# Optimization experiments

Measured on AMD Instinct MI355X. Metric: run time of the kernel, lower is better.

The kernel has to match this reference:

```python
import jax, jax.numpy as jnp
import numpy as np


def setup_inputs() -> dict:
    key = jax.random.key(0)
    ks = jax.random.split(key, 8)
    B, IN, H, OUT = 8192, 1024, 2048, 1024
    SIGMA_MIN, SIGMA_MAX, PHASE = 0.9, 0.999, 2.0 * np.pi
    # recurrence decay params, initialized as in the torch module
    rng = np.random.RandomState(0)
    u1 = rng.random_sample(H)
    u2 = rng.random_sample(H)
    v = -0.5 * np.log(u1 * (SIGMA_MAX ** 2 - SIGMA_MIN ** 2) + SIGMA_MIN ** 2)
    theta = u2 * PHASE
    scale_b = 1.0 / np.sqrt(IN)
    scale_c = 1.0 / np.sqrt(H)
    return {
        "x": jax.random.normal(ks[0], (B, IN), dtype=jnp.float32),
        "h_prev": jax.random.normal(ks[1], (B, H), dtype=jnp.float32),
        "Br": jax.random.normal(ks[2], (H, IN), dtype=jnp.float32) * scale_b,
        "Bi": jax.random.normal(ks[3], (H, IN), dtype=jnp.float32) * scale_b,
        "Cr": jax.random.normal(ks[4], (OUT, H), dtype=jnp.float32) * scale_c,
        "Ci": jax.random.normal(ks[5], (OUT, H), dtype=jnp.float32) * scale_c,
        "v_log": jnp.asarray(np.log(v), dtype=jnp.float32),
        "theta_log": jnp.asarray(np.log(theta), dtype=jnp.float32),
    }


def reference(x, h_prev, Br, Bi, Cr, Ci, v_log, theta_log):
    # effective diagonal recurrence weight w = exp(-exp(v_log) + i*exp(theta_log))
    mag = jnp.exp(-jnp.exp(v_log))            # [H]
    ang = jnp.exp(theta_log)                  # [H]
    wr = mag * jnp.cos(ang)
    wi = mag * jnp.sin(ang)
    # h = B(x) + h_prev * w  (h_prev is real -> imag part comes only from wi)
    # complexLinear on real x: real = x@Br^T, imag = x@Bi^T
    hr = jnp.einsum('bi,hi->bh', x, Br) + h_prev * wr   # [B,H]
    hi = jnp.einsum('bi,hi->bh', x, Bi) + h_prev * wi   # [B,H]
    # out = Re(C(h)) = hr@Cr^T - hi@Ci^T
    out = jnp.einsum('bh,oh->bo', hr, Cr) - jnp.einsum('bh,oh->bo', hi, Ci)
    return out
```

## Files before the change

### kernel.cpp

```cpp
#include <hip/hip_runtime.h>
#include <stdint.h>

typedef unsigned short u16;
typedef short bf16x8 __attribute__((ext_vector_type(8)));
typedef float f32x4 __attribute__((ext_vector_type(4)));

typedef void as1_void __attribute__((address_space(1)));
typedef void as3_void __attribute__((address_space(3)));

__device__ inline u16 f32_to_bf16(float f) {
    uint32_t u = __builtin_bit_cast(uint32_t, f);
    u += 0x7fffu + ((u >> 16) & 1u);
    return (u16)(u >> 16);
}

__device__ inline void gld_lds16(const void* g, void* l) {
    __builtin_amdgcn_global_load_lds((as1_void*)g, (as3_void*)l, 16, 0, 0);
}


__global__ void prep_w_kernel(const float* __restrict__ v_log,
                              const float* __restrict__ theta_log,
                              float* __restrict__ wfull, int H) {
    int h = blockIdx.x * blockDim.x + threadIdx.x;
    if (h < H) {
        float mag = expf(-expf(v_log[h]));
        float ang = expf(theta_log[h]);
        wfull[h]     = mag * cosf(ang);
        wfull[h + H] = mag * sinf(ang);
    }
}

__global__ void pack_ccat_kernel(const float* __restrict__ Cr,
                                 const float* __restrict__ Ci,
                                 u16* __restrict__ Ccat, int total4) {
    int i = blockIdx.x * blockDim.x + threadIdx.x;
    if (i >= total4) return;
    int e = i * 4;
    int o = e >> 12;
    int k = e & 4095;
    float4 f; float s;
    if (k < 2048) { f = *(const float4*)(Cr + (size_t)o * 2048 + k);          s =  1.f; }
    else          { f = *(const float4*)(Ci + (size_t)o * 2048 + (k - 2048)); s = -1.f; }
    ushort4 u;
    u.x = f32_to_bf16(s * f.x); u.y = f32_to_bf16(s * f.y);
    u.z = f32_to_bf16(s * f.z); u.w = f32_to_bf16(s * f.w);
    ((ushort4*)Ccat)[i] = u;
}

__global__ void transpose_cast_kernel(const float* __restrict__ Br,
                                      const float* __restrict__ Bi,
                                      u16* __restrict__ Bcat) {
    __shared__ float t[32][33];
    const float* src = blockIdx.z ? Bi : Br;
    int colOff = blockIdx.z ? 2048 : 0;
    int c0 = blockIdx.x * 32, r0 = blockIdx.y * 32;
    int tx = threadIdx.x, ty = threadIdx.y;
#pragma unroll
    for (int j = 0; j < 4; j++)
        t[ty + j * 8][tx] = src[(size_t)(r0 + ty + j * 8) * 1024 + c0 + tx];
    __syncthreads();
#pragma unroll
    for (int j = 0; j < 4; j++)
        Bcat[(size_t)(c0 + ty + j * 8) * 4096 + colOff + r0 + tx] =
            f32_to_bf16(t[tx][ty + j * 8]);
}

__global__ void cast_f32_bf16_kernel(const float* __restrict__ src,
                                     u16* __restrict__ dst, int n4) {
    int i = blockIdx.x * blockDim.x + threadIdx.x;
    if (i < n4) {
        float4 f = ((const float4*)src)[i];
        ushort4 o;
        o.x = f32_to_bf16(f.x); o.y = f32_to_bf16(f.y);
        o.z = f32_to_bf16(f.z); o.w = f32_to_bf16(f.w);
        ((ushort4*)dst)[i] = o;
    }
}

__global__ void reduce_cw_kernel(const float* __restrict__ partials,
                                 const float* __restrict__ Cr, const float* __restrict__ Ci,
                                 const float* __restrict__ wfull,
                                 u16* __restrict__ Wmain, u16* __restrict__ Cwbf) {
    const int n4_red = 1024 * 1024 / 4;
    const int n4_cw  = 1024 * 2048 / 4;
    int i = blockIdx.x * blockDim.x + threadIdx.x;
    if (i < n4_red) {
        int e = i * 4;
        float4 s = *(const float4*)(partials + e);
#pragma unroll
        for (int z = 1; z < 4; z++) {
            float4 p = *(const float4*)(partials + ((size_t)z << 20) + e);
            s.x += p.x; s.y += p.y; s.z += p.z; s.w += p.w;
        }
        ushort4 u;
        u.x = f32_to_bf16(s.x); u.y = f32_to_bf16(s.y);
        u.z = f32_to_bf16(s.z); u.w = f32_to_bf16(s.w);
        ((ushort4*)Wmain)[i] = u;
    } else if (i < n4_red + n4_cw) {
        int j = i - n4_red;
        int e = j * 4;
        int o = e >> 11;
        int h = e & 2047;
        float4 cr = *(const float4*)(Cr + (size_t)o * 2048 + h);
        float4 ci = *(const float4*)(Ci + (size_t)o * 2048 + h);
        float4 wr = *(const float4*)(wfull + h);
        float4 wi = *(const float4*)(wfull + 2048 + h);
        ushort4 u;
        u.x = f32_to_bf16(cr.x * wr.x - ci.x * wi.x);
        u.y = f32_to_bf16(cr.y * wr.y - ci.y * wi.y);
        u.z = f32_to_bf16(cr.z * wr.z - ci.z * wi.z);
        u.w = f32_to_bf16(cr.w * wr.w - ci.w * wi.w);
        ((ushort4*)Cwbf)[j] = u;
    }
}


__global__ __launch_bounds__(256)
void gemm_splitk_kernel(const u16* __restrict__ A, const u16* __restrict__ B,
                        float* __restrict__ partials)
{
    __shared__ __align__(16) u16 ldsA[128 * 32];
    __shared__ __align__(16) u16 ldsB[128 * 32];
    const int K = 4096;

    const int tid = threadIdx.x, wid = tid >> 6, lane = tid & 63;
    const int quad = lane >> 4, l16 = lane & 15;
    const int wm = wid >> 1, wn = wid & 1;
    const int bm = blockIdx.y, bn = blockIdx.x, bz = blockIdx.z;
    const int kb = bz * 1024;

    const int c0 = wid * 128 + lane, c1 = c0 + 64;
    const int r0 = c0 >> 2, o0 = (c0 & 3) * 8;
    const int r1 = c1 >> 2, o1 = (c1 & 3) * 8;

    const u16* gA0 = A + (size_t)(bm * 128 + r0) * K + o0 + kb;
    const u16* gA1 = A + (size_t)(bm * 128 + r1) * K + o1 + kb;
    const u16* gB0 = B + (size_t)(bn * 128 + r0) * K + o0 + kb;
    const u16* gB1 = B + (size_t)(bn * 128 + r1) * K + o1 + kb;
    u16* lA0 = ldsA + c0 * 8; u16* lA1 = ldsA + c1 * 8;
    u16* lB0 = ldsB + c0 * 8; u16* lB1 = ldsB + c1 * 8;

    const f32x4 fz = {0.f, 0.f, 0.f, 0.f};
    f32x4 acc[4][4];
#pragma unroll
    for (int i = 0; i < 4; i++)
#pragma unroll
        for (int j = 0; j < 4; j++) acc[i][j] = fz;

    for (int k0 = 0; k0 < 1024; k0 += 32) {
        __syncthreads();
        gld_lds16(gA0 + k0, lA0);
        gld_lds16(gA1 + k0, lA1);
        gld_lds16(gB0 + k0, lB0);
        gld_lds16(gB1 + k0, lB1);
        __syncthreads();
        bf16x8 af[4], bfr[4];
#pragma unroll
        for (int i = 0; i < 4; i++)
            af[i] = *(const bf16x8*)(ldsA + (wm * 64 + i * 16 + l16) * 32 + quad * 8);
#pragma unroll
        for (int j = 0; j < 4; j++)
            bfr[j] = *(const bf16x8*)(ldsB + (wn * 64 + j * 16 + l16) * 32 + quad * 8);
#pragma unroll
        for (int i = 0; i < 4; i++)
#pragma unroll
            for (int j = 0; j < 4; j++)
                acc[i][j] = __builtin_amdgcn_mfma_f32_16x16x32_bf16(af[i], bfr[j], acc[i][j], 0, 0, 0);
    }

    float* P = partials + ((size_t)bz << 20);
    const int gm = bm * 128 + wm * 64, gn = bn * 128 + wn * 64;
#pragma unroll
    for (int i = 0; i < 4; i++)
#pragma unroll
        for (int j = 0; j < 4; j++) {
            int col = gn + j * 16 + l16;
#pragma unroll
            for (int r = 0; r < 4; r++)
                P[(size_t)(gm + i * 16 + quad * 4 + r) * 1024 + col] = acc[i][j][r];
        }
}


__global__ __launch_bounds__(256)
void gemm_main_kernel(const u16* __restrict__ Axb, const u16* __restrict__ Ahb,
                      const u16* __restrict__ Bw,  const u16* __restrict__ Bcw,
                      float* __restrict__ out)
{
    __shared__ __align__(16) u16 ldsA[128 * 32];
    __shared__ __align__(16) u16 ldsB[128 * 32];

    const int tid = threadIdx.x, wid = tid >> 6, lane = tid & 63;
    const int quad = lane >> 4, l16 = lane & 15;
    const int wm = wid >> 1, wn = wid & 1;
    const int bm = blockIdx.y, bn = blockIdx.x;

    const int c0 = wid * 128 + lane, c1 = c0 + 64;
    const int r0 = c0 >> 2, o0 = (c0 & 3) * 8;
    const int r1 = c1 >> 2, o1 = (c1 & 3) * 8;
    u16* lA0 = ldsA + c0 * 8; u16* lA1 = ldsA + c1 * 8;
    u16* lB0 = ldsB + c0 * 8; u16* lB1 = ldsB + c1 * 8;

    const f32x4 fz = {0.f, 0.f, 0.f, 0.f};
    f32x4 acc[4][4];
#pragma unroll
    for (int i = 0; i < 4; i++)
#pragma unroll
        for (int j = 0; j < 4; j++) acc[i][j] = fz;

#pragma unroll 1
    for (int phase = 0; phase < 2; phase++) {
        const u16* Ap = phase ? Ahb : Axb;
        const u16* Bp = phase ? Bcw : Bw;
        const int KS = phase ? 2048 : 1024;
        const u16* gA0 = Ap + (size_t)(bm * 128 + r0) * KS + o0;
        const u16* gA1 = Ap + (size_t)(bm * 128 + r1) * KS + o1;
        const u16* gB0 = Bp + (size_t)(bn * 128 + r0) * KS + o0;
        const u16* gB1 = Bp + (size_t)(bn * 128 + r1) * KS + o1;
        for (int k0 = 0; k0 < KS; k0 += 32) {
            __syncthreads();
            gld_lds16(gA0 + k0, lA0);
            gld_lds16(gA1 + k0, lA1);
            gld_lds16(gB0 + k0, lB0);
            gld_lds16(gB1 + k0, lB1);
            __syncthreads();
            bf16x8 af[4], bfr[4];
#pragma unroll
            for (int i = 0; i < 4; i++)
                af[i] = *(const bf16x8*)(ldsA + (wm * 64 + i * 16 + l16) * 32 + quad * 8);
#pragma unroll
            for (int j = 0; j < 4; j++)
                bfr[j] = *(const bf16x8*)(ldsB + (wn * 64 + j * 16 + l16) * 32 + quad * 8);
#pragma unroll
            for (int i = 0; i < 4; i++)
#pragma unroll
                for (int j = 0; j < 4; j++)
                    acc[i][j] = __builtin_amdgcn_mfma_f32_16x16x32_bf16(af[i], bfr[j], acc[i][j], 0, 0, 0);
        }
    }

    const int gm = bm * 128 + wm * 64, gn = bn * 128 + wn * 64;
#pragma unroll
    for (int i = 0; i < 4; i++)
#pragma unroll
        for (int j = 0; j < 4; j++) {
            int col = gn + j * 16 + l16;
#pragma unroll
            for (int r = 0; r < 4; r++)
                out[(size_t)(gm + i * 16 + quad * 4 + r) * 1024 + col] = acc[i][j][r];
        }
}


extern "C" void kernel_launch(void* const* d_in, const int* in_sizes, int n_in,
                              void* d_out, int out_size, void* d_ws, size_t ws_size,
                              hipStream_t stream)
{
    const float* x      = (const float*)d_in[0];
    const float* h_prev = (const float*)d_in[1];
    const float* Br     = (const float*)d_in[2];
    const float* Bi     = (const float*)d_in[3];
    const float* Cr     = (const float*)d_in[4];
    const float* Ci     = (const float*)d_in[5];
    const float* v_log  = (const float*)d_in[6];
    const float* th_log = (const float*)d_in[7];
    float* out = (float*)d_out;

    const size_t MB = 1024 * 1024;
    size_t need = 48 * MB + 2 * MB + 4 * MB + 4096 * 4;
    if (ws_size < need) return;

    char* ws = (char*)d_ws;
    u16*   Ccat     = (u16*)ws;
    u16*   Bcat     = (u16*)(ws + 8 * MB);
    float* partials = (float*)(ws + 16 * MB);
    u16*   x_bf     = (u16*)ws;
    u16*   hp_bf    = (u16*)(ws + 16 * MB);
    u16*   Wmain    = (u16*)(ws + 48 * MB);
    u16*   Cwbf     = (u16*)(ws + 50 * MB);
    float* wfull    = (float*)(ws + 54 * MB);

    prep_w_kernel<<<8, 256, 0, stream>>>(v_log, th_log, wfull, 2048);
    pack_ccat_kernel<<<4096, 256, 0, stream>>>(Cr, Ci, Ccat, 1024 * 4096 / 4);
    transpose_cast_kernel<<<dim3(32, 64, 2), dim3(32, 8), 0, stream>>>(Br, Bi, Bcat);
    gemm_splitk_kernel<<<dim3(8, 8, 4), 256, 0, stream>>>(Ccat, Bcat, partials);
    reduce_cw_kernel<<<3072, 256, 0, stream>>>(partials, Cr, Ci, wfull, Wmain, Cwbf);
    cast_f32_bf16_kernel<<<8192, 256, 0, stream>>>(x, x_bf, 8192 * 1024 / 4);
    cast_f32_bf16_kernel<<<16384, 256, 0, stream>>>(h_prev, hp_bf, 8192 * 2048 / 4);
    gemm_main_kernel<<<dim3(8, 64), 256, 0, stream>>>(x_bf, hp_bf, Wmain, Cwbf, out);
}
```

Measured before the change: 282.4 us.

## Widen GEMM K-tile to 64 with XOR-swizzled LDS, deeper split-K, fused casts

Both GEMM kernels now stage 64-wide K tiles in LDS instead of 32, which halves the number of barrier pairs per K step. The LDS layout uses an XOR swizzle of 16-byte chunks by row so that fragment reads avoid bank conflicts. The weight-precompute split-K GEMM goes from 4 to 8 splits, giving more blocks, and the reduction is adjusted to sum 8 partials. The two cast kernels are merged into one launch, and the main GEMM uses a 1D grid with M-fastest block order. The costs are double the LDS per block, which may lower occupancy, and more partial-sum traffic in the reduction.

```diff
diff --git a/kernel.cpp b/kernel.cpp
--- a/kernel.cpp
+++ b/kernel.cpp
@@ -17,6 +17,7 @@
 __device__ inline void gld_lds16(const void* g, void* l) {
     __builtin_amdgcn_global_load_lds((as1_void*)g, (as3_void*)l, 16, 0, 0);
 }
+
 
 
 __global__ void prep_w_kernel(const float* __restrict__ v_log,
@@ -66,16 +67,16 @@
             f32_to_bf16(t[tx][ty + j * 8]);
 }
 
-__global__ void cast_f32_bf16_kernel(const float* __restrict__ src,
-                                     u16* __restrict__ dst, int n4) {
+__global__ void cast_both_kernel(const float* __restrict__ x,
+                                 const float* __restrict__ h_prev,
+                                 u16* __restrict__ dst) {
+    const int n4x = 8192 * 1024 / 4;
     int i = blockIdx.x * blockDim.x + threadIdx.x;
-    if (i < n4) {
-        float4 f = ((const float4*)src)[i];
-        ushort4 o;
-        o.x = f32_to_bf16(f.x); o.y = f32_to_bf16(f.y);
-        o.z = f32_to_bf16(f.z); o.w = f32_to_bf16(f.w);
-        ((ushort4*)dst)[i] = o;
-    }
+    float4 f = (i < n4x) ? ((const float4*)x)[i] : ((const float4*)h_prev)[i - n4x];
+    ushort4 o;
+    o.x = f32_to_bf16(f.x); o.y = f32_to_bf16(f.y);
+    o.z = f32_to_bf16(f.z); o.w = f32_to_bf16(f.w);
+    ((ushort4*)dst)[i] = o;
 }
 
 __global__ void reduce_cw_kernel(const float* __restrict__ partials,
@@ -89,7 +90,7 @@
         int e = i * 4;
         float4 s = *(const float4*)(partials + e);
 #pragma unroll
-        for (int z = 1; z < 4; z++) {
+        for (int z = 1; z < 8; z++) {
             float4 p = *(const float4*)(partials + ((size_t)z << 20) + e);
             s.x += p.x; s.y += p.y; s.z += p.z; s.w += p.w;
         }
@@ -120,26 +121,28 @@
 void gemm_splitk_kernel(const u16* __restrict__ A, const u16* __restrict__ B,
                         float* __restrict__ partials)
 {
-    __shared__ __align__(16) u16 ldsA[128 * 32];
-    __shared__ __align__(16) u16 ldsB[128 * 32];
+    __shared__ __align__(16) u16 ldsA[128 * 64];
+    __shared__ __align__(16) u16 ldsB[128 * 64];
     const int K = 4096;
 
     const int tid = threadIdx.x, wid = tid >> 6, lane = tid & 63;
     const int quad = lane >> 4, l16 = lane & 15;
     const int wm = wid >> 1, wn = wid & 1;
     const int bm = blockIdx.y, bn = blockIdx.x, bz = blockIdx.z;
-    const int kb = bz * 1024;
-
-    const int c0 = wid * 128 + lane, c1 = c0 + 64;
-    const int r0 = c0 >> 2, o0 = (c0 & 3) * 8;
-    const int r1 = c1 >> 2, o1 = (c1 & 3) * 8;
-
-    const u16* gA0 = A + (size_t)(bm * 128 + r0) * K + o0 + kb;
-    const u16* gA1 = A + (size_t)(bm * 128 + r1) * K + o1 + kb;
-    const u16* gB0 = B + (size_t)(bn * 128 + r0) * K + o0 + kb;
-    const u16* gB1 = B + (size_t)(bn * 128 + r1) * K + o1 + kb;
-    u16* lA0 = ldsA + c0 * 8; u16* lA1 = ldsA + c1 * 8;
-    u16* lB0 = ldsB + c0 * 8; u16* lB1 = ldsB + c1 * 8;
+    const int kb = bz * 512;
+
+    const u16* gA[4]; const u16* gB[4];
+    u16 *lA[4], *lB[4];
+#pragma unroll
+    for (int t = 0; t < 4; t++) {
+        int s = wid * 256 + t * 64 + lane;
+        int sr = s >> 3;
+        int sj = (s & 7) ^ (sr & 7);
+        lA[t] = ldsA + s * 8;
+        lB[t] = ldsB + s * 8;
+        gA[t] = A + (size_t)(bm * 128 + sr) * K + sj * 8 + kb;
+        gB[t] = B + (size_t)(bn * 128 + sr) * K + sj * 8 + kb;
+    }
 
     const f32x4 fz = {0.f, 0.f, 0.f, 0.f};
     f32x4 acc[4][4];
@@ -148,25 +151,33 @@
 #pragma unroll
         for (int j = 0; j < 4; j++) acc[i][j] = fz;
 
-    for (int k0 = 0; k0 < 1024; k0 += 32) {
+    for (int k0 = 0; k0 < 512; k0 += 64) {
         __syncthreads();
-        gld_lds16(gA0 + k0, lA0);
-        gld_lds16(gA1 + k0, lA1);
-        gld_lds16(gB0 + k0, lB0);
-        gld_lds16(gB1 + k0, lB1);
+#pragma unroll
+        for (int t = 0; t < 4; t++) {
+            gld_lds16(gA[t] + k0, lA[t]);
+            gld_lds16(gB[t] + k0, lB[t]);
+        }
         __syncthreads();
-        bf16x8 af[4], bfr[4];
-#pragma unroll
-        for (int i = 0; i < 4; i++)
-            af[i] = *(const bf16x8*)(ldsA + (wm * 64 + i * 16 + l16) * 32 + quad * 8);
-#pragma unroll
-        for (int j = 0; j < 4; j++)
-            bfr[j] = *(const bf16x8*)(ldsB + (wn * 64 + j * 16 + l16) * 32 + quad * 8);
-#pragma unroll
-        for (int i = 0; i < 4; i++)
-#pragma unroll
-            for (int j = 0; j < 4; j++)
-                acc[i][j] = __builtin_amdgcn_mfma_f32_16x16x32_bf16(af[i], bfr[j], acc[i][j], 0, 0, 0);
+#pragma unroll
+        for (int ks = 0; ks < 2; ks++) {
+            bf16x8 af[4], bfr[4];
+#pragma unroll
+            for (int i = 0; i < 4; i++) {
+                int r = wm * 64 + i * 16 + l16;
+                af[i] = *(const bf16x8*)(ldsA + (r * 8 + ((ks * 4 + quad) ^ (r & 7))) * 8);
+            }
+#pragma unroll
+            for (int j = 0; j < 4; j++) {
+                int r = wn * 64 + j * 16 + l16;
+                bfr[j] = *(const bf16x8*)(ldsB + (r * 8 + ((ks * 4 + quad) ^ (r & 7))) * 8);
+            }
+#pragma unroll
+            for (int i = 0; i < 4; i++)
+#pragma unroll
+                for (int j = 0; j < 4; j++)
+                    acc[i][j] = __builtin_amdgcn_mfma_f32_16x16x32_bf16(af[i], bfr[j], acc[i][j], 0, 0, 0);
+        }
     }
 
     float* P = partials + ((size_t)bz << 20);
@@ -188,19 +199,25 @@
                       const u16* __restrict__ Bw,  const u16* __restrict__ Bcw,
                       float* __restrict__ out)
 {
-    __shared__ __align__(16) u16 ldsA[128 * 32];
-    __shared__ __align__(16) u16 ldsB[128 * 32];
+    __shared__ __align__(16) u16 ldsA[128 * 64];
+    __shared__ __align__(16) u16 ldsB[128 * 64];
 
     const int tid = threadIdx.x, wid = tid >> 6, lane = tid & 63;
     const int quad = lane >> 4, l16 = lane & 15;
     const int wm = wid >> 1, wn = wid & 1;
-    const int bm = blockIdx.y, bn = blockIdx.x;
-
-    const int c0 = wid * 128 + lane, c1 = c0 + 64;
-    const int r0 = c0 >> 2, o0 = (c0 & 3) * 8;
-    const int r1 = c1 >> 2, o1 = (c1 & 3) * 8;
-    u16* lA0 = ldsA + c0 * 8; u16* lA1 = ldsA + c1 * 8;
-    u16* lB0 = ldsB + c0 * 8; u16* lB1 = ldsB + c1 * 8;
+    const int id = blockIdx.x;
+    const int bm = id & 63, bn = id >> 6;
+
+    int srow[4], sj[4];
+    u16 *lA[4], *lB[4];
+#pragma unroll
+    for (int t = 0; t < 4; t++) {
+        int s = wid * 256 + t * 64 + lane;
+        srow[t] = s >> 3;
+        sj[t] = (s & 7) ^ (srow[t] & 7);
+        lA[t] = ldsA + s * 8;
+        lB[t] = ldsB + s * 8;
+    }
 
     const f32x4 fz = {0.f, 0.f, 0.f, 0.f};
     f32x4 acc[4][4];
@@ -214,29 +231,39 @@
         const u16* Ap = phase ? Ahb : Axb;
         const u16* Bp = phase ? Bcw : Bw;
         const int KS = phase ? 2048 : 1024;
-        const u16* gA0 = Ap + (size_t)(bm * 128 + r0) * KS + o0;
-        const u16* gA1 = Ap + (size_t)(bm * 128 + r1) * KS + o1;
-        const u16* gB0 = Bp + (size_t)(bn * 128 + r0) * KS + o0;
-        const u16* gB1 = Bp + (size_t)(bn * 128 + r1) * KS + o1;
-        for (int k0 = 0; k0 < KS; k0 += 32) {
+        const u16* gA[4]; const u16* gB[4];
+#pragma unroll
+        for (int t = 0; t < 4; t++) {
+            gA[t] = Ap + (size_t)(bm * 128 + srow[t]) * KS + sj[t] * 8;
+            gB[t] = Bp + (size_t)(bn * 128 + srow[t]) * KS + sj[t] * 8;
+        }
+        for (int k0 = 0; k0 < KS; k0 += 64) {
             __syncthreads();
-            gld_lds16(gA0 + k0, lA0);
-            gld_lds16(gA1 + k0, lA1);
-            gld_lds16(gB0 + k0, lB0);
-            gld_lds16(gB1 + k0, lB1);
+#pragma unroll
+            for (int t = 0; t < 4; t++) {
+                gld_lds16(gA[t] + k0, lA[t]);
+                gld_lds16(gB[t] + k0, lB[t]);
+            }
             __syncthreads();
-            bf16x8 af[4], bfr[4];
-#pragma unroll
-            for (int i = 0; i < 4; i++)
-                af[i] = *(const bf16x8*)(ldsA + (wm * 64 + i * 16 + l16) * 32 + quad * 8);
-#pragma unroll
-            for (int j = 0; j < 4; j++)
-                bfr[j] = *(const bf16x8*)(ldsB + (wn * 64 + j * 16 + l16) * 32 + quad * 8);
-#pragma unroll
-            for (int i = 0; i < 4; i++)
-#pragma unroll
-                for (int j = 0; j < 4; j++)
-                    acc[i][j] = __builtin_amdgcn_mfma_f32_16x16x32_bf16(af[i], bfr[j], acc[i][j], 0, 0, 0);
+#pragma unroll
+            for (int ks = 0; ks < 2; ks++) {
+                bf16x8 af[4], bfr[4];
+#pragma unroll
+                for (int i = 0; i < 4; i++) {
+                    int r = wm * 64 + i * 16 + l16;
+                    af[i] = *(const bf16x8*)(ldsA + (r * 8 + ((ks * 4 + quad) ^ (r & 7))) * 8);
+                }
+#pragma unroll
+                for (int j = 0; j < 4; j++) {
+                    int r = wn * 64 + j * 16 + l16;
+                    bfr[j] = *(const bf16x8*)(ldsB + (r * 8 + ((ks * 4 + quad) ^ (r & 7))) * 8);
+                }
+#pragma unroll
+                for (int i = 0; i < 4; i++)
+#pragma unroll
+                    for (int j = 0; j < 4; j++)
+                        acc[i][j] = __builtin_amdgcn_mfma_f32_16x16x32_bf16(af[i], bfr[j], acc[i][j], 0, 0, 0);
+            }
         }
     }
 
@@ -268,7 +295,7 @@
     float* out = (float*)d_out;
 
     const size_t MB = 1024 * 1024;
-    size_t need = 48 * MB + 2 * MB + 4 * MB + 4096 * 4;
+    size_t need = 54 * MB + 4096 * 4;
     if (ws_size < need) return;
 
     char* ws = (char*)d_ws;
@@ -284,9 +311,8 @@
     prep_w_kernel<<<8, 256, 0, stream>>>(v_log, th_log, wfull, 2048);
     pack_ccat_kernel<<<4096, 256, 0, stream>>>(Cr, Ci, Ccat, 1024 * 4096 / 4);
     transpose_cast_kernel<<<dim3(32, 64, 2), dim3(32, 8), 0, stream>>>(Br, Bi, Bcat);
-    gemm_splitk_kernel<<<dim3(8, 8, 4), 256, 0, stream>>>(Ccat, Bcat, partials);
+    gemm_splitk_kernel<<<dim3(8, 8, 8), 256, 0, stream>>>(Ccat, Bcat, partials);
     reduce_cw_kernel<<<3072, 256, 0, stream>>>(partials, Cr, Ci, wfull, Wmain, Cwbf);
-    cast_f32_bf16_kernel<<<8192, 256, 0, stream>>>(x, x_bf, 8192 * 1024 / 4);
-    cast_f32_bf16_kernel<<<16384, 256, 0, stream>>>(h_prev, hp_bf, 8192 * 2048 / 4);
-    gemm_main_kernel<<<dim3(8, 64), 256, 0, stream>>>(x_bf, hp_bf, Wmain, Cwbf, out);
-}
+    cast_both_kernel<<<24576, 256, 0, stream>>>(x, h_prev, x_bf);
+    gemm_main_kernel<<<512, 256, 0, stream>>>(x_bf, hp_bf, Wmain, Cwbf, out);
+}
```

Measured after the change: 250.9 us. 11.1% less time.
